# Kernel optimization log

Hardware: AMD Instinct MI355X
Metric: run time of the kernel (lower is better)

The kernel has to match this reference:

```python
import jax, jax.numpy as jnp
import numpy as np

N = 50000      # nodes
E = 800000     # edges
F_IN = 256     # input node features
H = 64         # hidden_dim
C = 10         # num_classes
G = 64         # graphs in batch


def setup_inputs() -> dict:
    key = jax.random.key(0)
    ks = jax.random.split(key, 10)
    x = jax.random.normal(ks[0], (N, F_IN), dtype=jnp.float32)
    edge_index = jax.random.randint(ks[1], (2, E), 0, N, dtype=jnp.int64)
    batch = jnp.sort(jax.random.randint(ks[2], (N,), 0, G, dtype=jnp.int64))
    def glorot(k, fan_in, fan_out):
        return jax.random.normal(k, (fan_in, fan_out), dtype=jnp.float32) / jnp.sqrt(jnp.float32(fan_in))
    return {
        "x": x,
        "edge_index": edge_index,
        "batch": batch,
        "W1": glorot(ks[3], F_IN, H), "b1": jnp.zeros((H,), jnp.float32),
        "W2": glorot(ks[4], H, H),    "b2": jnp.zeros((H,), jnp.float32),
        "W3": glorot(ks[5], H, H),    "b3": jnp.zeros((H,), jnp.float32),
        "lin_W": glorot(ks[6], H, C), "lin_b": jnp.zeros((C,), jnp.float32),
    }


def reference(x, edge_index, batch, W1, b1, W2, b2, W3, b3, lin_W, lin_b):
    src, dst = edge_index[0], edge_index[1]
    # GCN normalization with self-loops: deg counts (A + I) in-degree
    deg = jax.ops.segment_sum(jnp.ones((E,), x.dtype), dst, num_segments=N) + 1.0
    dis = jax.lax.rsqrt(deg)                       # deg^{-1/2}, [N]
    edge_norm = dis[src] * dis[dst]                # [E]
    self_norm = dis * dis                          # [N] (self-loop weight)

    def gcn_conv_relu(h, W, b):
        h = h @ W                                  # [N, H]
        msg = h[src] * edge_norm[:, None]          # gather + scale, [E, H]
        agg = jax.ops.segment_sum(msg, dst, num_segments=N)
        agg = agg + h * self_norm[:, None]         # self-loop contribution
        return jax.nn.relu(agg + b)                # dropout is identity in eval

    h = gcn_conv_relu(x, W1, b1)
    h = gcn_conv_relu(h, W2, b2)
    h = gcn_conv_relu(h, W3, b3)

    # global mean pool over graphs
    counts = jax.ops.segment_sum(jnp.ones((N,), h.dtype), batch, num_segments=G)
    pooled = jax.ops.segment_sum(h, batch, num_segments=G) / jnp.maximum(counts, 1.0)[:, None]
    return pooled @ lin_W + lin_b                  # [G, C]
```

## Files before the change

kernel.cpp:

```cpp
#include <hip/hip_runtime.h>

#define N_NODES 50000
#define N_EDGES 800000
#define F_INPUT 256
#define HDIM 64
#define NCLS 10
#define NGRAPH 64

#define BSHIFT 7
#define NBUCK 391
#define SCAP 4096

typedef float f32x4v __attribute__((ext_vector_type(4)));
typedef short bf16x8 __attribute__((ext_vector_type(8)));

union B8U { uint4 q; bf16x8 v; };

__device__ __forceinline__ float bflo(unsigned v) { return __uint_as_float(v << 16); }
__device__ __forceinline__ float bfhi(unsigned v) { return __uint_as_float(v & 0xFFFF0000u); }
__device__ __forceinline__ unsigned f2b2(float a, float b) {
    unsigned x = __float_as_uint(a); x = (x + 0x7FFF + ((x >> 16) & 1)) >> 16;
    unsigned y = __float_as_uint(b); y = (y + 0x7FFF + ((y >> 16) & 1)) >> 16;
    return x | (y << 16);
}

__device__ __forceinline__ void split2(float x0, float x1, unsigned& h, unsigned& l) {
    unsigned u0 = __float_as_uint(x0), u1 = __float_as_uint(x1);
    unsigned m0 = u0 & 0xFFFF0000u, m1 = u1 & 0xFFFF0000u;
    h = (u0 >> 16) | m1;
    float r0 = x0 - __uint_as_float(m0);
    float r1 = x1 - __uint_as_float(m1);
    l = (__float_as_uint(r0) >> 16) | (__float_as_uint(r1) & 0xFFFF0000u);
}

__global__ __launch_bounds__(256) void k_part(const int* __restrict__ src,
                                              const int* __restrict__ dst,
                                              int* __restrict__ bcnt,
                                              int* __restrict__ stage, int E) {
    __shared__ int cnt[NBUCK];
    __shared__ int base[NBUCK];
    const int tid = threadIdx.x;
    const int e0 = blockIdx.x * 4096;
    int pb[16], pv[16];
    for (int t = tid; t < NBUCK; t += 256) cnt[t] = 0;
    __syncthreads();
#pragma unroll
    for (int j = 0; j < 16; ++j) {
        int e = e0 + j * 256 + tid;
        if (e < E) {
            int s = src[e], d = dst[e];
            pb[j] = d >> BSHIFT;
            pv[j] = (s << BSHIFT) | (d & 127);
            atomicAdd(&cnt[pb[j]], 1);
        } else pb[j] = -1;
    }
    __syncthreads();
    for (int t = tid; t < NBUCK; t += 256) {
        int c = cnt[t];
        base[t] = c ? atomicAdd(&bcnt[t], c) : 0;
        cnt[t] = 0;
    }
    __syncthreads();
#pragma unroll
    for (int j = 0; j < 16; ++j) {
        if (pb[j] >= 0) {
            int r = base[pb[j]] + atomicAdd(&cnt[pb[j]], 1);
            if (r < SCAP) stage[pb[j] * SCAP + r] = pv[j];
        }
    }
}

__global__ __launch_bounds__(256) void k_csr(const int* __restrict__ stage,
                                             const int* __restrict__ bcnt,
                                             int* __restrict__ degi,
                                             float* __restrict__ dis,
                                             int* __restrict__ off,
                                             int* __restrict__ eadj, int n) {
    __shared__ int cnt[128];
    __shared__ int loc[128];
    __shared__ int lcur[128];
    __shared__ int ebuf[SCAP];
    const int b = blockIdx.x;
    const int tid = threadIdx.x;
    const int n0 = b << BSHIFT;
    const int nn = min(128, n - n0);
    const int sb = b * SCAP;
    const int len = min(bcnt[b], SCAP);
    if (tid < 128) cnt[tid] = 0;
    __syncthreads();
    for (int j = tid; j < len; j += 256) atomicAdd(&cnt[stage[sb + j] & 127], 1);
    __syncthreads();
    if (tid < nn) {
        int dg = cnt[tid];
        degi[n0 + tid] = dg;
        dis[n0 + tid] = rsqrtf((float)(dg + 1));
    }
    if (tid < 128) loc[tid] = cnt[tid];
    __syncthreads();
    for (int d = 1; d < 128; d <<= 1) {
        int x = 0;
        if (tid < 128 && tid >= d) x = loc[tid - d];
        __syncthreads();
        if (tid < 128) loc[tid] += x;
        __syncthreads();
    }
    if (tid < 128) {
        int ex = loc[tid] - cnt[tid];
        if (tid < nn) off[n0 + tid] = sb + ex;
        lcur[tid] = ex;
    }
    __syncthreads();
    for (int j = tid; j < len; j += 256) {
        int p = stage[sb + j];
        int rk = atomicAdd(&lcur[p & 127], 1);
        ebuf[rk] = p >> BSHIFT;
    }
    __syncthreads();
    for (int j = tid; j < len; j += 256) eadj[sb + j] = ebuf[j];
}

__global__ __launch_bounds__(256) void k_prepW(const float* __restrict__ W1,
                                               const float* __restrict__ W2,
                                               const float* __restrict__ W3,
                                               uint4* __restrict__ Bf1,
                                               uint4* __restrict__ Bf2,
                                               uint4* __restrict__ Bf3) {
    int s = blockIdx.x * 256 + threadIdx.x;
    const float* W; uint4* out; int local, KS;
    if (s < 2048)      { W = W1; out = Bf1; local = s;        KS = 8; }
    else if (s < 2560) { W = W2; out = Bf2; local = s - 2048; KS = 2; }
    else               { W = W3; out = Bf3; local = s - 2560; KS = 2; }
    const int lane = local & 63;
    const int t    = (local >> 6) & 3;
    const int ks   = local >> 8;
    const int kb   = ks * 32 + ((lane >> 4) << 3);
    const int col  = t * 16 + (lane & 15);
    unsigned h[4], l[4];
#pragma unroll
    for (int j = 0; j < 4; ++j) {
        float x0 = W[(size_t)(kb + 2 * j) * HDIM + col];
        float x1 = W[(size_t)(kb + 2 * j + 1) * HDIM + col];
        split2(x0, x1, h[j], l[j]);
    }
    out[(ks * 4 + t) * 64 + lane]          = make_uint4(h[0], h[1], h[2], h[3]);
    out[((KS + ks) * 4 + t) * 64 + lane]   = make_uint4(l[0], l[1], l[2], l[3]);
}

__global__ __launch_bounds__(256) void k_gemm_mf(const float* __restrict__ A,
                                                 const uint4* __restrict__ Bf,
                                                 unsigned short* __restrict__ C,
                                                 int n, int lda, int ktn) {
    const int tid = threadIdx.x;
    const int ln  = tid & 63;
    const int wv  = tid >> 6;
    const int m   = ln & 15;
    const int kg  = ln >> 4;
    const int grow = blockIdx.x * 64 + wv * 16 + m;
    const float* ar = A + (size_t)min(grow, n - 1) * lda + kg * 8;

    f32x4v acc[4];
#pragma unroll
    for (int t = 0; t < 4; ++t)
#pragma unroll
        for (int j = 0; j < 4; ++j) acc[t][j] = 0.0f;

    float4 c0 = *(const float4*)(ar);
    float4 c1 = *(const float4*)(ar + 4);

    for (int ks = 0; ks < ktn; ++ks) {
        const int kn = (ks + 1 < ktn) ? (ks + 1) * 32 : 0;
        float4 p0 = *(const float4*)(ar + kn);
        float4 p1 = *(const float4*)(ar + kn + 4);

        const uint4* bp = Bf + (size_t)ks * 256 + ln;
        const uint4* bq = Bf + (size_t)(ktn + ks) * 256 + ln;
        B8U bh0, bh1, bh2, bh3, bl0, bl1, bl2, bl3;
        bh0.q = bp[0];   bh1.q = bp[64];  bh2.q = bp[128]; bh3.q = bp[192];
        bl0.q = bq[0];   bl1.q = bq[64];  bl2.q = bq[128]; bl3.q = bq[192];

        B8U ah, al;
        split2(c0.x, c0.y, ah.q.x, al.q.x);
        split2(c0.z, c0.w, ah.q.y, al.q.y);
        split2(c1.x, c1.y, ah.q.z, al.q.z);
        split2(c1.z, c1.w, ah.q.w, al.q.w);

        acc[0] = __builtin_amdgcn_mfma_f32_16x16x32_bf16(bh0.v, ah.v, acc[0], 0, 0, 0);
        acc[1] = __builtin_amdgcn_mfma_f32_16x16x32_bf16(bh1.v, ah.v, acc[1], 0, 0, 0);
        acc[2] = __builtin_amdgcn_mfma_f32_16x16x32_bf16(bh2.v, ah.v, acc[2], 0, 0, 0);
        acc[3] = __builtin_amdgcn_mfma_f32_16x16x32_bf16(bh3.v, ah.v, acc[3], 0, 0, 0);
        acc[0] = __builtin_amdgcn_mfma_f32_16x16x32_bf16(bl0.v, ah.v, acc[0], 0, 0, 0);
        acc[1] = __builtin_amdgcn_mfma_f32_16x16x32_bf16(bl1.v, ah.v, acc[1], 0, 0, 0);
        acc[2] = __builtin_amdgcn_mfma_f32_16x16x32_bf16(bl2.v, ah.v, acc[2], 0, 0, 0);
        acc[3] = __builtin_amdgcn_mfma_f32_16x16x32_bf16(bl3.v, ah.v, acc[3], 0, 0, 0);
        acc[0] = __builtin_amdgcn_mfma_f32_16x16x32_bf16(bh0.v, al.v, acc[0], 0, 0, 0);
        acc[1] = __builtin_amdgcn_mfma_f32_16x16x32_bf16(bh1.v, al.v, acc[1], 0, 0, 0);
        acc[2] = __builtin_amdgcn_mfma_f32_16x16x32_bf16(bh2.v, al.v, acc[2], 0, 0, 0);
        acc[3] = __builtin_amdgcn_mfma_f32_16x16x32_bf16(bh3.v, al.v, acc[3], 0, 0, 0);

        c0 = p0; c1 = p1;
    }

    if (grow < n) {
#pragma unroll
        for (int t = 0; t < 4; ++t) {
            uint2 p;
            p.x = f2b2(acc[t][0], acc[t][1]);
            p.y = f2b2(acc[t][2], acc[t][3]);
            *(uint2*)(C + (size_t)grow * HDIM + t * 16 + kg * 4) = p;
        }
    }
}

__global__ __launch_bounds__(256) void k_gemm_mb(const unsigned short* __restrict__ A,
                                                 const uint4* __restrict__ Bf,
                                                 unsigned short* __restrict__ C, int n) {
    const int tid = threadIdx.x;
    const int ln  = tid & 63;
    const int wv  = tid >> 6;
    const int m   = ln & 15;
    const int kg  = ln >> 4;
    const int grow = blockIdx.x * 64 + wv * 16 + m;
    const unsigned short* ar = A + (size_t)min(grow, n - 1) * HDIM + kg * 8;

    f32x4v acc[4];
#pragma unroll
    for (int t = 0; t < 4; ++t)
#pragma unroll
        for (int j = 0; j < 4; ++j) acc[t][j] = 0.0f;

#pragma unroll
    for (int ks = 0; ks < 2; ++ks) {
        B8U af;
        af.q = *(const uint4*)(ar + ks * 32);
        const uint4* bp = Bf + ks * 256 + ln;
        const uint4* bq = Bf + (2 + ks) * 256 + ln;
        B8U bh0, bh1, bh2, bh3, bl0, bl1, bl2, bl3;
        bh0.q = bp[0];  bh1.q = bp[64];  bh2.q = bp[128]; bh3.q = bp[192];
        bl0.q = bq[0];  bl1.q = bq[64];  bl2.q = bq[128]; bl3.q = bq[192];

        acc[0] = __builtin_amdgcn_mfma_f32_16x16x32_bf16(bh0.v, af.v, acc[0], 0, 0, 0);
        acc[1] = __builtin_amdgcn_mfma_f32_16x16x32_bf16(bh1.v, af.v, acc[1], 0, 0, 0);
        acc[2] = __builtin_amdgcn_mfma_f32_16x16x32_bf16(bh2.v, af.v, acc[2], 0, 0, 0);
        acc[3] = __builtin_amdgcn_mfma_f32_16x16x32_bf16(bh3.v, af.v, acc[3], 0, 0, 0);
        acc[0] = __builtin_amdgcn_mfma_f32_16x16x32_bf16(bl0.v, af.v, acc[0], 0, 0, 0);
        acc[1] = __builtin_amdgcn_mfma_f32_16x16x32_bf16(bl1.v, af.v, acc[1], 0, 0, 0);
        acc[2] = __builtin_amdgcn_mfma_f32_16x16x32_bf16(bl2.v, af.v, acc[2], 0, 0, 0);
        acc[3] = __builtin_amdgcn_mfma_f32_16x16x32_bf16(bl3.v, af.v, acc[3], 0, 0, 0);
    }

    if (grow < n) {
#pragma unroll
        for (int t = 0; t < 4; ++t) {
            uint2 p;
            p.x = f2b2(acc[t][0], acc[t][1]);
            p.y = f2b2(acc[t][2], acc[t][3]);
            *(uint2*)(C + (size_t)grow * HDIM + t * 16 + kg * 4) = p;
        }
    }
}

__global__ __launch_bounds__(256) void k_gather_b(const unsigned short* __restrict__ h,
                                                  const int* __restrict__ off,
                                                  const int* __restrict__ degi,
                                                  const int* __restrict__ eadj,
                                                  const float* __restrict__ dis,
                                                  const float* __restrict__ bias,
                                                  unsigned short* __restrict__ out, int n) {
    int t = blockIdx.x * 256 + threadIdx.x;
    int i = t >> 3;
    if (i >= n) return;
    int q = (t & 7) * 8;
    float di = dis[i];
    int e0 = off[i];
    int e1 = e0 + degi[i];
    float a0 = 0.f, a1 = 0.f, a2 = 0.f, a3 = 0.f, a4 = 0.f, a5 = 0.f, a6 = 0.f, a7 = 0.f;
    float g0 = 0.f, g1 = 0.f, g2 = 0.f, g3 = 0.f, g4 = 0.f, g5 = 0.f, g6 = 0.f, g7 = 0.f;
    int e = e0;
    for (; e + 1 < e1; e += 2) {
        int s0 = eadj[e];
        int s1 = eadj[e + 1];
        uint4 u0 = *(const uint4*)(h + (size_t)s0 * HDIM + q);
        uint4 u1 = *(const uint4*)(h + (size_t)s1 * HDIM + q);
        float w0 = dis[s0] * di;
        float w1 = dis[s1] * di;
        a0 = fmaf(bflo(u0.x), w0, a0); a1 = fmaf(bfhi(u0.x), w0, a1);
        a2 = fmaf(bflo(u0.y), w0, a2); a3 = fmaf(bfhi(u0.y), w0, a3);
        a4 = fmaf(bflo(u0.z), w0, a4); a5 = fmaf(bfhi(u0.z), w0, a5);
        a6 = fmaf(bflo(u0.w), w0, a6); a7 = fmaf(bfhi(u0.w), w0, a7);
        g0 = fmaf(bflo(u1.x), w1, g0); g1 = fmaf(bfhi(u1.x), w1, g1);
        g2 = fmaf(bflo(u1.y), w1, g2); g3 = fmaf(bfhi(u1.y), w1, g3);
        g4 = fmaf(bflo(u1.z), w1, g4); g5 = fmaf(bfhi(u1.z), w1, g5);
        g6 = fmaf(bflo(u1.w), w1, g6); g7 = fmaf(bfhi(u1.w), w1, g7);
    }
    if (e < e1) {
        int s0 = eadj[e];
        uint4 u0 = *(const uint4*)(h + (size_t)s0 * HDIM + q);
        float w0 = dis[s0] * di;
        a0 = fmaf(bflo(u0.x), w0, a0); a1 = fmaf(bfhi(u0.x), w0, a1);
        a2 = fmaf(bflo(u0.y), w0, a2); a3 = fmaf(bfhi(u0.y), w0, a3);
        a4 = fmaf(bflo(u0.z), w0, a4); a5 = fmaf(bfhi(u0.z), w0, a5);
        a6 = fmaf(bflo(u0.w), w0, a6); a7 = fmaf(bfhi(u0.w), w0, a7);
    }
    a0 += g0; a1 += g1; a2 += g2; a3 += g3;
    a4 += g4; a5 += g5; a6 += g6; a7 += g7;
    float sn = di * di;
    uint4 us = *(const uint4*)(h + (size_t)i * HDIM + q);
    float4 bl = *(const float4*)(bias + q);
    float4 bh = *(const float4*)(bias + q + 4);
    a0 = fmaxf(fmaf(bflo(us.x), sn, a0) + bl.x, 0.f);
    a1 = fmaxf(fmaf(bfhi(us.x), sn, a1) + bl.y, 0.f);
    a2 = fmaxf(fmaf(bflo(us.y), sn, a2) + bl.z, 0.f);
    a3 = fmaxf(fmaf(bfhi(us.y), sn, a3) + bl.w, 0.f);
    a4 = fmaxf(fmaf(bflo(us.z), sn, a4) + bh.x, 0.f);
    a5 = fmaxf(fmaf(bfhi(us.z), sn, a5) + bh.y, 0.f);
    a6 = fmaxf(fmaf(bflo(us.w), sn, a6) + bh.z, 0.f);
    a7 = fmaxf(fmaf(bfhi(us.w), sn, a7) + bh.w, 0.f);
    uint4 o;
    o.x = f2b2(a0, a1); o.y = f2b2(a2, a3);
    o.z = f2b2(a4, a5); o.w = f2b2(a6, a7);
    *(uint4*)(out + (size_t)i * HDIM + q) = o;
}

__global__ __launch_bounds__(256) void k_gather_pool(const unsigned short* __restrict__ h,
                                                     const int* __restrict__ off,
                                                     const int* __restrict__ degi,
                                                     const int* __restrict__ eadj,
                                                     const float* __restrict__ dis,
                                                     const float* __restrict__ bias,
                                                     const int* __restrict__ batch,
                                                     float* __restrict__ pooled, int n) {
    __shared__ float sp[NGRAPH][HDIM];
    const int tid = threadIdx.x;
    int t = blockIdx.x * 256 + tid;
    int i = t >> 3;
    const bool valid = (i < n);
    int q = (t & 7) * 8;
    const int i0 = (blockIdx.x * 256) >> 3;
    const int i1 = min(i0 + 32, n);
    const int gmin = batch[min(i0, n - 1)];
    const int gmax = batch[i1 - 1];
    for (int j = tid; j < NGRAPH * HDIM; j += 256) ((float*)sp)[j] = 0.f;
    __syncthreads();
    if (valid) {
        float di = dis[i];
        int e0 = off[i];
        int e1 = e0 + degi[i];
        float a0 = 0.f, a1 = 0.f, a2 = 0.f, a3 = 0.f, a4 = 0.f, a5 = 0.f, a6 = 0.f, a7 = 0.f;
        float g0 = 0.f, g1 = 0.f, g2 = 0.f, g3 = 0.f, g4 = 0.f, g5 = 0.f, g6 = 0.f, g7 = 0.f;
        int e = e0;
        for (; e + 1 < e1; e += 2) {
            int s0 = eadj[e];
            int s1 = eadj[e + 1];
            uint4 u0 = *(const uint4*)(h + (size_t)s0 * HDIM + q);
            uint4 u1 = *(const uint4*)(h + (size_t)s1 * HDIM + q);
            float w0 = dis[s0] * di;
            float w1 = dis[s1] * di;
            a0 = fmaf(bflo(u0.x), w0, a0); a1 = fmaf(bfhi(u0.x), w0, a1);
            a2 = fmaf(bflo(u0.y), w0, a2); a3 = fmaf(bfhi(u0.y), w0, a3);
            a4 = fmaf(bflo(u0.z), w0, a4); a5 = fmaf(bfhi(u0.z), w0, a5);
            a6 = fmaf(bflo(u0.w), w0, a6); a7 = fmaf(bfhi(u0.w), w0, a7);
            g0 = fmaf(bflo(u1.x), w1, g0); g1 = fmaf(bfhi(u1.x), w1, g1);
            g2 = fmaf(bflo(u1.y), w1, g2); g3 = fmaf(bfhi(u1.y), w1, g3);
            g4 = fmaf(bflo(u1.z), w1, g4); g5 = fmaf(bfhi(u1.z), w1, g5);
            g6 = fmaf(bflo(u1.w), w1, g6); g7 = fmaf(bfhi(u1.w), w1, g7);
        }
        if (e < e1) {
            int s0 = eadj[e];
            uint4 u0 = *(const uint4*)(h + (size_t)s0 * HDIM + q);
            float w0 = dis[s0] * di;
            a0 = fmaf(bflo(u0.x), w0, a0); a1 = fmaf(bfhi(u0.x), w0, a1);
            a2 = fmaf(bflo(u0.y), w0, a2); a3 = fmaf(bfhi(u0.y), w0, a3);
            a4 = fmaf(bflo(u0.z), w0, a4); a5 = fmaf(bfhi(u0.z), w0, a5);
            a6 = fmaf(bflo(u0.w), w0, a6); a7 = fmaf(bfhi(u0.w), w0, a7);
        }
        a0 += g0; a1 += g1; a2 += g2; a3 += g3;
        a4 += g4; a5 += g5; a6 += g6; a7 += g7;
        float sn = di * di;
        uint4 us = *(const uint4*)(h + (size_t)i * HDIM + q);
        float4 bl = *(const float4*)(bias + q);
        float4 bh = *(const float4*)(bias + q + 4);
        a0 = fmaxf(fmaf(bflo(us.x), sn, a0) + bl.x, 0.f);
        a1 = fmaxf(fmaf(bfhi(us.x), sn, a1) + bl.y, 0.f);
        a2 = fmaxf(fmaf(bflo(us.y), sn, a2) + bl.z, 0.f);
        a3 = fmaxf(fmaf(bfhi(us.y), sn, a3) + bl.w, 0.f);
        a4 = fmaxf(fmaf(bflo(us.z), sn, a4) + bh.x, 0.f);
        a5 = fmaxf(fmaf(bfhi(us.z), sn, a5) + bh.y, 0.f);
        a6 = fmaxf(fmaf(bflo(us.w), sn, a6) + bh.z, 0.f);
        a7 = fmaxf(fmaf(bfhi(us.w), sn, a7) + bh.w, 0.f);
        int g = batch[i];
        atomicAdd(&sp[g][q + 0], a0); atomicAdd(&sp[g][q + 1], a1);
        atomicAdd(&sp[g][q + 2], a2); atomicAdd(&sp[g][q + 3], a3);
        atomicAdd(&sp[g][q + 4], a4); atomicAdd(&sp[g][q + 5], a5);
        atomicAdd(&sp[g][q + 6], a6); atomicAdd(&sp[g][q + 7], a7);
    }
    __syncthreads();
    int rows = gmax - gmin + 1;
    for (int j = tid; j < rows * HDIM; j += 256) {
        int r = j >> 6, c = j & 63;
        float v = sp[gmin + r][c];
        if (v != 0.f) atomicAdd(&pooled[(gmin + r) * HDIM + c], v);
    }
}

__global__ __launch_bounds__(640) void k_head(const float* __restrict__ pooled,
                                              const int* __restrict__ batch,
                                              const float* __restrict__ linW,
                                              const float* __restrict__ linb,
                                              float* __restrict__ out, int n) {
    int t = threadIdx.x;
    if (t >= NGRAPH * NCLS) return;
    int g = t / NCLS;
    int c = t - g * NCLS;
    int lo = 0, hi = n;
    while (lo < hi) { int m = (lo + hi) >> 1; if (batch[m] < g) lo = m + 1; else hi = m; }
    int s = lo;
    lo = 0; hi = n;
    while (lo < hi) { int m = (lo + hi) >> 1; if (batch[m] < g + 1) lo = m + 1; else hi = m; }
    float inv = 1.0f / fmaxf((float)(lo - s), 1.0f);
    float acc = linb[c];
#pragma unroll
    for (int k = 0; k < HDIM; ++k)
        acc = fmaf(pooled[g * HDIM + k] * inv, linW[k * NCLS + c], acc);
    out[g * NCLS + c] = acc;
}

extern "C" void kernel_launch(void* const* d_in, const int* in_sizes, int n_in,
                              void* d_out, int out_size, void* d_ws, size_t ws_size,
                              hipStream_t stream) {
    (void)in_sizes; (void)n_in; (void)out_size; (void)ws_size;
    const float* x    = (const float*)d_in[0];
    const int*   ei   = (const int*)d_in[1];
    const int*   batch= (const int*)d_in[2];
    const float* W1   = (const float*)d_in[3];
    const float* b1   = (const float*)d_in[4];
    const float* W2   = (const float*)d_in[5];
    const float* b2   = (const float*)d_in[6];
    const float* W3   = (const float*)d_in[7];
    const float* b3   = (const float*)d_in[8];
    const float* linW = (const float*)d_in[9];
    const float* linb = (const float*)d_in[10];
    float* out = (float*)d_out;

    const int N = N_NODES, E = N_EDGES;
    const int* src = ei;
    const int* dst = ei + E;

    char* ws = (char*)d_ws;
    unsigned short* hA = (unsigned short*)ws; ws += (size_t)N * HDIM * 2;
    unsigned short* hB = (unsigned short*)ws; ws += (size_t)N * HDIM * 2;
    float* dis    = (float*)ws; ws += (size_t)N * 4;
    int*   eadj   = (int*)ws;   ws += (size_t)NBUCK * SCAP * 4;
    int*   stage  = (int*)ws;   ws += (size_t)NBUCK * SCAP * 4;
    int*   degi   = (int*)ws;   ws += (size_t)N * 4;
    int*   off    = (int*)ws;   ws += (size_t)N * 4;
    int*   bcnt   = (int*)ws;   ws += ((size_t)NBUCK * 4 + 15) & ~(size_t)15;
    float* pooled = (float*)ws; ws += (size_t)NGRAPH * HDIM * 4;
    uint4* Bf1    = (uint4*)ws; ws += (size_t)2 * 8 * 4 * 64 * 16;
    uint4* Bf2    = (uint4*)ws; ws += (size_t)2 * 2 * 4 * 64 * 16;
    uint4* Bf3    = (uint4*)ws; ws += (size_t)2 * 2 * 4 * 64 * 16;

    const int nbE = (E + 4095) / 4096;
    const int gb  = (N + 63) / 64;
    const int ngth = (N * 8 + 255) / 256;

    hipMemsetAsync(bcnt, 0, (size_t)NBUCK * 4, stream);
    hipMemsetAsync(pooled, 0, (size_t)NGRAPH * HDIM * 4, stream);
    k_prepW<<<12, 256, 0, stream>>>(W1, W2, W3, Bf1, Bf2, Bf3);
    k_part<<<nbE, 256, 0, stream>>>(src, dst, bcnt, stage, E);
    k_csr<<<NBUCK, 256, 0, stream>>>(stage, bcnt, degi, dis, off, eadj, N);

    k_gemm_mf<<<gb, 256, 0, stream>>>(x, Bf1, hA, N, F_INPUT, 8);
    k_gather_b<<<ngth, 256, 0, stream>>>(hA, off, degi, eadj, dis, b1, hB, N);
    k_gemm_mb<<<gb, 256, 0, stream>>>(hB, Bf2, hA, N);
    k_gather_b<<<ngth, 256, 0, stream>>>(hA, off, degi, eadj, dis, b2, hB, N);
    k_gemm_mb<<<gb, 256, 0, stream>>>(hB, Bf3, hA, N);
    k_gather_pool<<<ngth, 256, 0, stream>>>(hA, off, degi, eadj, dis, b3, batch, pooled, N);
    k_head<<<1, 640, 0, stream>>>(pooled, batch, linW, linb, out, N);
}
```

Baseline: 246.3 us.

## Fold source-side degree scaling into GEMM epilogue and pack CSR ranges

The symmetric normalization is factored so each GEMM scales its output row by dis[row], and the gather applies dis[i] once at the end. This removes the per-edge random dis[src] load and multiply, so the inner loop becomes plain bf16 adds. Offset, end and dis are packed into one int4 per node so a single load replaces three, and the edge loop is unrolled to four gathers per iteration. The pre-scaled bf16 rounding changes numerics slightly.

```diff
diff --git a/kernel.cpp b/kernel.cpp
--- a/kernel.cpp
+++ b/kernel.cpp
@@ -32,6 +32,12 @@
     float r1 = x1 - __uint_as_float(m1);
     l = (__float_as_uint(r0) >> 16) | (__float_as_uint(r1) & 0xFFFF0000u);
 }
+
+#define ADD8(b, u)                                    \
+    b##0 += bflo(u.x); b##1 += bfhi(u.x);             \
+    b##2 += bflo(u.y); b##3 += bfhi(u.y);             \
+    b##4 += bflo(u.z); b##5 += bfhi(u.z);             \
+    b##6 += bflo(u.w); b##7 += bfhi(u.w);
 
 __global__ __launch_bounds__(256) void k_part(const int* __restrict__ src,
                                               const int* __restrict__ dst,
@@ -72,9 +78,8 @@
 
 __global__ __launch_bounds__(256) void k_csr(const int* __restrict__ stage,
                                              const int* __restrict__ bcnt,
-                                             int* __restrict__ degi,
                                              float* __restrict__ dis,
-                                             int* __restrict__ off,
+                                             int4* __restrict__ rng,
                                              int* __restrict__ eadj, int n) {
     __shared__ int cnt[128];
     __shared__ int loc[128];
@@ -90,11 +95,6 @@
     __syncthreads();
     for (int j = tid; j < len; j += 256) atomicAdd(&cnt[stage[sb + j] & 127], 1);
     __syncthreads();
-    if (tid < nn) {
-        int dg = cnt[tid];
-        degi[n0 + tid] = dg;
-        dis[n0 + tid] = rsqrtf((float)(dg + 1));
-    }
     if (tid < 128) loc[tid] = cnt[tid];
     __syncthreads();
     for (int d = 1; d < 128; d <<= 1) {
@@ -106,7 +106,12 @@
     }
     if (tid < 128) {
         int ex = loc[tid] - cnt[tid];
-        if (tid < nn) off[n0 + tid] = sb + ex;
+        if (tid < nn) {
+            int dg = cnt[tid];
+            float di = rsqrtf((float)(dg + 1));
+            dis[n0 + tid] = di;
+            rng[n0 + tid] = make_int4(sb + ex, sb + ex + dg, __float_as_int(di), 0);
+        }
         lcur[tid] = ex;
     }
     __syncthreads();
@@ -148,6 +153,7 @@
 
 __global__ __launch_bounds__(256) void k_gemm_mf(const float* __restrict__ A,
                                                  const uint4* __restrict__ Bf,
+                                                 const float* __restrict__ dis,
                                                  unsigned short* __restrict__ C,
                                                  int n, int lda, int ktn) {
     const int tid = threadIdx.x;
@@ -201,11 +207,12 @@
     }
 
     if (grow < n) {
+        const float di = dis[grow];
 #pragma unroll
         for (int t = 0; t < 4; ++t) {
             uint2 p;
-            p.x = f2b2(acc[t][0], acc[t][1]);
-            p.y = f2b2(acc[t][2], acc[t][3]);
+            p.x = f2b2(acc[t][0] * di, acc[t][1] * di);
+            p.y = f2b2(acc[t][2] * di, acc[t][3] * di);
             *(uint2*)(C + (size_t)grow * HDIM + t * 16 + kg * 4) = p;
         }
     }
@@ -213,6 +220,7 @@
 
 __global__ __launch_bounds__(256) void k_gemm_mb(const unsigned short* __restrict__ A,
                                                  const uint4* __restrict__ Bf,
+                                                 const float* __restrict__ dis,
                                                  unsigned short* __restrict__ C, int n) {
     const int tid = threadIdx.x;
     const int ln  = tid & 63;
@@ -249,72 +257,65 @@
     }
 
     if (grow < n) {
+        const float di = dis[grow];
 #pragma unroll
         for (int t = 0; t < 4; ++t) {
             uint2 p;
-            p.x = f2b2(acc[t][0], acc[t][1]);
-            p.y = f2b2(acc[t][2], acc[t][3]);
+            p.x = f2b2(acc[t][0] * di, acc[t][1] * di);
+            p.y = f2b2(acc[t][2] * di, acc[t][3] * di);
             *(uint2*)(C + (size_t)grow * HDIM + t * 16 + kg * 4) = p;
         }
     }
 }
 
 __global__ __launch_bounds__(256) void k_gather_b(const unsigned short* __restrict__ h,
-                                                  const int* __restrict__ off,
-                                                  const int* __restrict__ degi,
                                                   const int* __restrict__ eadj,
-                                                  const float* __restrict__ dis,
+                                                  const int4* __restrict__ rng,
                                                   const float* __restrict__ bias,
                                                   unsigned short* __restrict__ out, int n) {
     int t = blockIdx.x * 256 + threadIdx.x;
     int i = t >> 3;
     if (i >= n) return;
-    int q = (t & 7) * 8;
-    float di = dis[i];
-    int e0 = off[i];
-    int e1 = e0 + degi[i];
+    const int q = (t & 7) * 8;
+    const int4 r = rng[i];
+    int e = r.x; const int e1 = r.y;
+    const float di = __int_as_float(r.z);
     float a0 = 0.f, a1 = 0.f, a2 = 0.f, a3 = 0.f, a4 = 0.f, a5 = 0.f, a6 = 0.f, a7 = 0.f;
     float g0 = 0.f, g1 = 0.f, g2 = 0.f, g3 = 0.f, g4 = 0.f, g5 = 0.f, g6 = 0.f, g7 = 0.f;
-    int e = e0;
-    for (; e + 1 < e1; e += 2) {
+#pragma unroll 2
+    for (; e + 3 < e1; e += 4) {
         int s0 = eadj[e];
         int s1 = eadj[e + 1];
+        int s2 = eadj[e + 2];
+        int s3 = eadj[e + 3];
         uint4 u0 = *(const uint4*)(h + (size_t)s0 * HDIM + q);
         uint4 u1 = *(const uint4*)(h + (size_t)s1 * HDIM + q);
-        float w0 = dis[s0] * di;
-        float w1 = dis[s1] * di;
-        a0 = fmaf(bflo(u0.x), w0, a0); a1 = fmaf(bfhi(u0.x), w0, a1);
-        a2 = fmaf(bflo(u0.y), w0, a2); a3 = fmaf(bfhi(u0.y), w0, a3);
-        a4 = fmaf(bflo(u0.z), w0, a4); a5 = fmaf(bfhi(u0.z), w0, a5);
-        a6 = fmaf(bflo(u0.w), w0, a6); a7 = fmaf(bfhi(u0.w), w0, a7);
-        g0 = fmaf(bflo(u1.x), w1, g0); g1 = fmaf(bfhi(u1.x), w1, g1);
-        g2 = fmaf(bflo(u1.y), w1, g2); g3 = fmaf(bfhi(u1.y), w1, g3);
-        g4 = fmaf(bflo(u1.z), w1, g4); g5 = fmaf(bfhi(u1.z), w1, g5);
-        g6 = fmaf(bflo(u1.w), w1, g6); g7 = fmaf(bfhi(u1.w), w1, g7);
-    }
-    if (e < e1) {
+        uint4 u2 = *(const uint4*)(h + (size_t)s2 * HDIM + q);
+        uint4 u3 = *(const uint4*)(h + (size_t)s3 * HDIM + q);
+        ADD8(a, u0)
+        ADD8(g, u1)
+        ADD8(a, u2)
+        ADD8(g, u3)
+    }
+    for (; e < e1; ++e) {
         int s0 = eadj[e];
         uint4 u0 = *(const uint4*)(h + (size_t)s0 * HDIM + q);
-        float w0 = dis[s0] * di;
-        a0 = fmaf(bflo(u0.x), w0, a0); a1 = fmaf(bfhi(u0.x), w0, a1);
-        a2 = fmaf(bflo(u0.y), w0, a2); a3 = fmaf(bfhi(u0.y), w0, a3);
-        a4 = fmaf(bflo(u0.z), w0, a4); a5 = fmaf(bfhi(u0.z), w0, a5);
-        a6 = fmaf(bflo(u0.w), w0, a6); a7 = fmaf(bfhi(u0.w), w0, a7);
-    }
+        ADD8(a, u0)
+    }
+    uint4 us = *(const uint4*)(h + (size_t)i * HDIM + q);
+    ADD8(a, us)
     a0 += g0; a1 += g1; a2 += g2; a3 += g3;
     a4 += g4; a5 += g5; a6 += g6; a7 += g7;
-    float sn = di * di;
-    uint4 us = *(const uint4*)(h + (size_t)i * HDIM + q);
     float4 bl = *(const float4*)(bias + q);
     float4 bh = *(const float4*)(bias + q + 4);
-    a0 = fmaxf(fmaf(bflo(us.x), sn, a0) + bl.x, 0.f);
-    a1 = fmaxf(fmaf(bfhi(us.x), sn, a1) + bl.y, 0.f);
-    a2 = fmaxf(fmaf(bflo(us.y), sn, a2) + bl.z, 0.f);
-    a3 = fmaxf(fmaf(bfhi(us.y), sn, a3) + bl.w, 0.f);
-    a4 = fmaxf(fmaf(bflo(us.z), sn, a4) + bh.x, 0.f);
-    a5 = fmaxf(fmaf(bfhi(us.z), sn, a5) + bh.y, 0.f);
-    a6 = fmaxf(fmaf(bflo(us.w), sn, a6) + bh.z, 0.f);
-    a7 = fmaxf(fmaf(bfhi(us.w), sn, a7) + bh.w, 0.f);
+    a0 = fmaxf(fmaf(a0, di, bl.x), 0.f);
+    a1 = fmaxf(fmaf(a1, di, bl.y), 0.f);
+    a2 = fmaxf(fmaf(a2, di, bl.z), 0.f);
+    a3 = fmaxf(fmaf(a3, di, bl.w), 0.f);
+    a4 = fmaxf(fmaf(a4, di, bh.x), 0.f);
+    a5 = fmaxf(fmaf(a5, di, bh.y), 0.f);
+    a6 = fmaxf(fmaf(a6, di, bh.z), 0.f);
+    a7 = fmaxf(fmaf(a7, di, bh.w), 0.f);
     uint4 o;
     o.x = f2b2(a0, a1); o.y = f2b2(a2, a3);
     o.z = f2b2(a4, a5); o.w = f2b2(a6, a7);
@@ -322,10 +323,8 @@
 }
 
 __global__ __launch_bounds__(256) void k_gather_pool(const unsigned short* __restrict__ h,
-                                                     const int* __restrict__ off,
-                                                     const int* __restrict__ degi,
                                                      const int* __restrict__ eadj,
-                                                     const float* __restrict__ dis,
+                                                     const int4* __restrict__ rng,
                                                      const float* __restrict__ bias,
                                                      const int* __restrict__ batch,
                                                      float* __restrict__ pooled, int n) {
@@ -342,51 +341,45 @@
     for (int j = tid; j < NGRAPH * HDIM; j += 256) ((float*)sp)[j] = 0.f;
     __syncthreads();
     if (valid) {
-        float di = dis[i];
-        int e0 = off[i];
-        int e1 = e0 + degi[i];
+        const int4 r = rng[i];
+        int e = r.x; const int e1 = r.y;
+        const float di = __int_as_float(r.z);
         float a0 = 0.f, a1 = 0.f, a2 = 0.f, a3 = 0.f, a4 = 0.f, a5 = 0.f, a6 = 0.f, a7 = 0.f;
         float g0 = 0.f, g1 = 0.f, g2 = 0.f, g3 = 0.f, g4 = 0.f, g5 = 0.f, g6 = 0.f, g7 = 0.f;
-        int e = e0;
-        for (; e + 1 < e1; e += 2) {
+#pragma unroll 2
+        for (; e + 3 < e1; e += 4) {
             int s0 = eadj[e];
             int s1 = eadj[e + 1];
+            int s2 = eadj[e + 2];
+            int s3 = eadj[e + 3];
             uint4 u0 = *(const uint4*)(h + (size_t)s0 * HDIM + q);
             uint4 u1 = *(const uint4*)(h + (size_t)s1 * HDIM + q);
-            float w0 = dis[s0] * di;
-            float w1 = dis[s1] * di;
-            a0 = fmaf(bflo(u0.x), w0, a0); a1 = fmaf(bfhi(u0.x), w0, a1);
-            a2 = fmaf(bflo(u0.y), w0, a2); a3 = fmaf(bfhi(u0.y), w0, a3);
-            a4 = fmaf(bflo(u0.z), w0, a4); a5 = fmaf(bfhi(u0.z), w0, a5);
-            a6 = fmaf(bflo(u0.w), w0, a6); a7 = fmaf(bfhi(u0.w), w0, a7);
-            g0 = fmaf(bflo(u1.x), w1, g0); g1 = fmaf(bfhi(u1.x), w1, g1);
-            g2 = fmaf(bflo(u1.y), w1, g2); g3 = fmaf(bfhi(u1.y), w1, g3);
-            g4 = fmaf(bflo(u1.z), w1, g4); g5 = fmaf(bfhi(u1.z), w1, g5);
-            g6 = fmaf(bflo(u1.w), w1, g6); g7 = fmaf(bfhi(u1.w), w1, g7);
-        }
-        if (e < e1) {
+            uint4 u2 = *(const uint4*)(h + (size_t)s2 * HDIM + q);
+            uint4 u3 = *(const uint4*)(h + (size_t)s3 * HDIM + q);
+            ADD8(a, u0)
+            ADD8(g, u1)
+            ADD8(a, u2)
+            ADD8(g, u3)
+        }
+        for (; e < e1; ++e) {
             int s0 = eadj[e];
             uint4 u0 = *(const uint4*)(h + (size_t)s0 * HDIM + q);
-            float w0 = dis[s0] * di;
-            a0 = fmaf(bflo(u0.x), w0, a0); a1 = fmaf(bfhi(u0.x), w0, a1);
-            a2 = fmaf(bflo(u0.y), w0, a2); a3 = fmaf(bfhi(u0.y), w0, a3);
-            a4 = fmaf(bflo(u0.z), w0, a4); a5 = fmaf(bfhi(u0.z), w0, a5);
-            a6 = fmaf(bflo(u0.w), w0, a6); a7 = fmaf(bfhi(u0.w), w0, a7);
-        }
+            ADD8(a, u0)
+        }
+        uint4 us = *(const uint4*)(h + (size_t)i * HDIM + q);
+        ADD8(a, us)
         a0 += g0; a1 += g1; a2 += g2; a3 += g3;
         a4 += g4; a5 += g5; a6 += g6; a7 += g7;
-        float sn = di * di;
-        uint4 us = *(const uint4*)(h + (size_t)i * HDIM + q);
         float4 bl = *(const float4*)(bias + q);
         float4 bh = *(const float4*)(bias + q + 4);
-        a0 = fmaxf(fmaf(bflo(us.x), sn, a0) + bl.x, 0.f);
-        a1 = fmaxf(fmaf(bfhi(us.x), sn, a1) + bl.y, 0.f);
-        a2 = fmaxf(fmaf(bflo(us.y), sn, a2) + bl.z, 0.f);
-        a3 = fmaxf(fmaf(bfhi(us.y), sn, a3) + bl.w, 0.f);
-        a4 = fmaxf(fmaf(bflo(us.z), sn, a4) + bh.x, 0.f);
-        a5 = fmaxf(fmaf(bfhi(us.z), sn, a5) + bh.y, 0.f);
-        a6 = fmaxf(fmaf(bflo(us.w), sn, a6) + bh.z, 0.f);
-        a7 = fmaxf(fmaf(bfhi(us.w), sn, a7) + bh.w, 0.f);
+        a0 = fmaxf(fmaf(a0, di, bl.x), 0.f);
+        a1 = fmaxf(fmaf(a1, di, bl.y), 0.f);
+        a2 = fmaxf(fmaf(a2, di, bl.z), 0.f);
+        a3 = fmaxf(fmaf(a3, di, bl.w), 0.f);
+        a4 = fmaxf(fmaf(a4, di, bh.x), 0.f);
+        a5 = fmaxf(fmaf(a5, di, bh.y), 0.f);
+        a6 = fmaxf(fmaf(a6, di, bh.z), 0.f);
+        a7 = fmaxf(fmaf(a7, di, bh.w), 0.f);
         int g = batch[i];
         atomicAdd(&sp[g][q + 0], a0); atomicAdd(&sp[g][q + 1], a1);
         atomicAdd(&sp[g][q + 2], a2); atomicAdd(&sp[g][q + 3], a3);
@@ -451,8 +444,7 @@
     float* dis    = (float*)ws; ws += (size_t)N * 4;
     int*   eadj   = (int*)ws;   ws += (size_t)NBUCK * SCAP * 4;
     int*   stage  = (int*)ws;   ws += (size_t)NBUCK * SCAP * 4;
-    int*   degi   = (int*)ws;   ws += (size_t)N * 4;
-    int*   off    = (int*)ws;   ws += (size_t)N * 4;
+    int4*  rng    = (int4*)ws;  ws += (size_t)N * 16;
     int*   bcnt   = (int*)ws;   ws += ((size_t)NBUCK * 4 + 15) & ~(size_t)15;
     float* pooled = (float*)ws; ws += (size_t)NGRAPH * HDIM * 4;
     uint4* Bf1    = (uint4*)ws; ws += (size_t)2 * 8 * 4 * 64 * 16;
@@ -467,13 +459,13 @@
     hipMemsetAsync(pooled, 0, (size_t)NGRAPH * HDIM * 4, stream);
     k_prepW<<<12, 256, 0, stream>>>(W1, W2, W3, Bf1, Bf2, Bf3);
     k_part<<<nbE, 256, 0, stream>>>(src, dst, bcnt, stage, E);
-    k_csr<<<NBUCK, 256, 0, stream>>>(stage, bcnt, degi, dis, off, eadj, N);
-
-    k_gemm_mf<<<gb, 256, 0, stream>>>(x, Bf1, hA, N, F_INPUT, 8);
-    k_gather_b<<<ngth, 256, 0, stream>>>(hA, off, degi, eadj, dis, b1, hB, N);
-    k_gemm_mb<<<gb, 256, 0, stream>>>(hB, Bf2, hA, N);
-    k_gather_b<<<ngth, 256, 0, stream>>>(hA, off, degi, eadj, dis, b2, hB, N);
-    k_gemm_mb<<<gb, 256, 0, stream>>>(hB, Bf3, hA, N);
-    k_gather_pool<<<ngth, 256, 0, stream>>>(hA, off, degi, eadj, dis, b3, batch, pooled, N);
+    k_csr<<<NBUCK, 256, 0, stream>>>(stage, bcnt, dis, rng, eadj, N);
+
+    k_gemm_mf<<<gb, 256, 0, stream>>>(x, Bf1, dis, hA, N, F_INPUT, 8);
+    k_gather_b<<<ngth, 256, 0, stream>>>(hA, eadj, rng, b1, hB, N);
+    k_gemm_mb<<<gb, 256, 0, stream>>>(hB, Bf2, dis, hA, N);
+    k_gather_b<<<ngth, 256, 0, stream>>>(hA, eadj, rng, b2, hB, N);
+    k_gemm_mb<<<gb, 256, 0, stream>>>(hB, Bf3, dis, hA, N);
+    k_gather_pool<<<ngth, 256, 0, stream>>>(hA, eadj, rng, b3, batch, pooled, N);
     k_head<<<1, 640, 0, stream>>>(pooled, batch, linW, linb, out, N);
 }
```

Result: no change. 248.2 us (+0.7%).
